# Kernel optimization log

Hardware: AMD Instinct MI355X
Metric: run time of the kernel (lower is better)

The kernel has to match this reference:

```python
import jax, jax.numpy as jnp
import numpy as np

TAU = 1.0
K_TAU = 1.0
MAX_K = 64


def setup_inputs() -> dict:
    key = jax.random.key(0)
    ks = jax.random.split(key, 6)
    B, S, D, H = 8, 4096, 1024, 2048
    token_embeddings = jax.random.normal(ks[0], (B, S, D), dtype=jnp.float32)
    W1 = jax.random.normal(ks[1], (D, H), dtype=jnp.float32) * (1.0 / np.sqrt(D))
    b1 = jnp.zeros((H,), dtype=jnp.float32)
    W2 = jax.random.normal(ks[2], (H, 1), dtype=jnp.float32) * (1.0 / np.sqrt(H))
    b2 = jnp.zeros((1,), dtype=jnp.float32)
    k_logits = jax.random.normal(ks[3], (MAX_K,), dtype=jnp.float32) * 0.02
    return {"token_embeddings": token_embeddings, "W1": W1, "b1": b1,
            "W2": W2, "b2": b2, "k_logits": k_logits}


def _gumbel(rng, shape):
    u = jax.random.uniform(rng, shape, minval=1e-08, maxval=1.0 - 1e-08)
    return -jnp.log(-jnp.log(u))


def reference(token_embeddings, W1, b1, W2, b2, k_logits):
    B, S, D = token_embeddings.shape
    # scorer: Dense -> relu -> Dense(1), squeeze -> [B, S]
    h = jax.nn.relu(jnp.einsum('bsd,dh->bsh', token_embeddings, W1) + b1)
    importance_logits = (jnp.einsum('bsh,ho->bso', h, W2) + b2)[..., 0]

    rng = jax.random.key(42)  # training rng
    rng1, rng2 = jax.random.split(rng)

    # learnable-k selection (training branch)
    k_gumbel = _gumbel(rng1, k_logits.shape)
    k_soft = jax.nn.softmax((k_logits + k_gumbel) / K_TAU)
    expected_k = jnp.sum(k_soft * jnp.arange(1, MAX_K + 1, dtype=k_soft.dtype))
    k_selected = jnp.argmax(k_soft) + 1  # traced int scalar

    # gumbel-softmax hard top-k over tokens
    perturbed = importance_logits + _gumbel(rng2, importance_logits.shape)
    soft_mask = jax.nn.softmax(perturbed / TAU, axis=-1)  # [B, S]
    # rank of each token (0 = smallest); top-k == rank >= S - k
    rank = jnp.argsort(jnp.argsort(soft_mask, axis=-1), axis=-1)
    hard_mask = (rank >= S - k_selected).astype(soft_mask.dtype)
    selection_mask = jax.lax.stop_gradient(hard_mask - soft_mask) + soft_mask

    filtered_embeddings = token_embeddings * selection_mask[..., None]
    return filtered_embeddings, selection_mask, expected_k
```

## Files before the change

### kernel.cpp

```cpp
#include <hip/hip_runtime.h>
#include <stdint.h>

#define B_BATCH 8
#define S_SEQ   4096
#define D_DIM   1024
#define H_DIM   2048
#define M_TOK   (B_BATCH * S_SEQ)
#define MAXK    64
#define NSPLIT  2

typedef unsigned int u32;
typedef unsigned short u16;
typedef unsigned long long u64;
typedef __attribute__((ext_vector_type(8))) short short8;
typedef __attribute__((ext_vector_type(4))) float f32x4;

#define GLOBAL_AS __attribute__((address_space(1)))
#define LDS_AS    __attribute__((address_space(3)))


#define TF_ROUND(x0, x1, r) { x0 += x1; x1 = ((x1 << r) | (x1 >> (32 - r))); x1 ^= x0; }

__device__ __forceinline__ void tf2x32(u32 k0, u32 k1, u32 x0, u32 x1, u32& o0, u32& o1) {
  u32 k2 = k0 ^ k1 ^ 0x1BD11BDAu;
  x0 += k0; x1 += k1;
  TF_ROUND(x0, x1, 13) TF_ROUND(x0, x1, 15) TF_ROUND(x0, x1, 26) TF_ROUND(x0, x1, 6)
  x0 += k1; x1 += k2 + 1u;
  TF_ROUND(x0, x1, 17) TF_ROUND(x0, x1, 29) TF_ROUND(x0, x1, 16) TF_ROUND(x0, x1, 24)
  x0 += k2; x1 += k0 + 2u;
  TF_ROUND(x0, x1, 13) TF_ROUND(x0, x1, 15) TF_ROUND(x0, x1, 26) TF_ROUND(x0, x1, 6)
  x0 += k0; x1 += k1 + 3u;
  TF_ROUND(x0, x1, 17) TF_ROUND(x0, x1, 29) TF_ROUND(x0, x1, 16) TF_ROUND(x0, x1, 24)
  x0 += k1; x1 += k2 + 4u;
  TF_ROUND(x0, x1, 13) TF_ROUND(x0, x1, 15) TF_ROUND(x0, x1, 26) TF_ROUND(x0, x1, 6)
  x0 += k2; x1 += k0 + 5u;
  o0 = x0; o1 = x1;
}

__device__ __forceinline__ void jax_subkeys(u32& r1a, u32& r1b, u32& r2a, u32& r2b) {
  tf2x32(0u, 42u, 0u, 0u, r1a, r1b);
  tf2x32(0u, 42u, 0u, 1u, r2a, r2b);
}

__device__ __forceinline__ u32 jax_bits32(u32 ka, u32 kb, u32 i) {
  u32 o0, o1;
  tf2x32(ka, kb, 0u, i, o0, o1);
  return o0 ^ o1;
}

__device__ __forceinline__ float jax_uniform_from_bits(u32 bits) {
  float f = __uint_as_float((bits >> 9) | 0x3f800000u) - 1.0f;
  float r = f + 1e-8f;
  return fmaxf(1e-8f, r);
}

__device__ __forceinline__ float gumbel_from_bits(u32 bits) {
  float u = jax_uniform_from_bits(bits);
  return -logf(-logf(u));
}

__device__ __forceinline__ u32 ordf(float v) {
  u32 b = __float_as_uint(v);
  return (b & 0x80000000u) ? ~b : (b | 0x80000000u);
}

__device__ __forceinline__ u64 shflx64(u64 v, int m) {
  unsigned lo = (unsigned)v, hi = (unsigned)(v >> 32);
  lo = (unsigned)__shfl_xor((int)lo, m);
  hi = (unsigned)__shfl_xor((int)hi, m);
  return ((u64)hi << 32) | lo;
}


__device__ __forceinline__ u16 f2bf_rn(float x) {
  u32 u = __float_as_uint(x);
  u32 r = u + 0x7fffu + ((u >> 16) & 1u);
  return (u16)(r >> 16);
}

__device__ __forceinline__ void split1(float x, u16& h, u16& lo) {
  h = f2bf_rn(x);
  float hf = __uint_as_float(((u32)h) << 16);
  lo = f2bf_rn(x - hf);
}


__global__ __launch_bounds__(256) void split_a_kernel(const float* __restrict__ x,
                                                      u16* __restrict__ hi,
                                                      u16* __restrict__ lo) {
  const size_t i = ((size_t)blockIdx.x * 256 + threadIdx.x) * 4;
  float4 v = *(const float4*)(x + i);
  u16 h0, h1, h2, h3, l0, l1, l2, l3;
  split1(v.x, h0, l0); split1(v.y, h1, l1); split1(v.z, h2, l2); split1(v.w, h3, l3);
  u64 hv = (u64)h0 | ((u64)h1 << 16) | ((u64)h2 << 32) | ((u64)h3 << 48);
  u64 lv = (u64)l0 | ((u64)l1 << 16) | ((u64)l2 << 32) | ((u64)l3 << 48);
  *(u64*)(hi + i) = hv;
  *(u64*)(lo + i) = lv;
}

__global__ __launch_bounds__(256) void split_w1t_kernel(const float* __restrict__ W1,
                                                        u16* __restrict__ bhi,
                                                        u16* __restrict__ blo) {
  __shared__ float tile[32][33];
  const int tx = threadIdx.x & 31, ty = threadIdx.x >> 5;
  const int n0 = blockIdx.x * 32, k0 = blockIdx.y * 32;
  #pragma unroll
  for (int r = 0; r < 4; ++r)
    tile[ty + r * 8][tx] = W1[(size_t)(k0 + ty + r * 8) * H_DIM + n0 + tx];
  __syncthreads();
  #pragma unroll
  for (int r = 0; r < 4; ++r) {
    const int n = n0 + ty + r * 8, k = k0 + tx;
    u16 h, l;
    split1(tile[tx][ty + r * 8], h, l);
    bhi[(size_t)n * D_DIM + k] = h;
    blo[(size_t)n * D_DIM + k] = l;
  }
}


__device__ __forceinline__ void stage16(const u16* g, u16* l) {
  __builtin_amdgcn_global_load_lds((const GLOBAL_AS u32*)g, (LDS_AS u32*)l, 16, 0, 0);
}

__global__ __launch_bounds__(256, 2) void scorer_mfma(
    const u16* __restrict__ Ahi, const u16* __restrict__ Alo,
    const u16* __restrict__ Bhi, const u16* __restrict__ Blo,
    const float* __restrict__ b1, const float* __restrict__ W2,
    float* __restrict__ pl) {
  __shared__ u16 smem[4 * 128 * 32];
  u16* sAhi = smem;
  u16* sAlo = smem + 4096;
  u16* sBhi = smem + 8192;
  u16* sBlo = smem + 12288;

  const int tid = threadIdx.x;
  const int w = tid >> 6;
  const int l = tid & 63;
  const int m0 = blockIdx.x * 128;
  const int nyb = blockIdx.y;

  const int rl0 = w * 32 + (l >> 2);
  const int rl1 = rl0 + 16;
  const int kloc0 = (((l & 3) ^ ((rl0 >> 1) & 3)) << 3);
  const int kloc1 = (((l & 3) ^ ((rl1 >> 1) & 3)) << 3);
  const int lb0 = (w * 32) * 32;
  const int lb1 = (w * 32 + 16) * 32;

  int a_off[4], b_off[4];
  #pragma unroll
  for (int i = 0; i < 4; ++i) {
    int row = ((w & 1) << 6) + i * 16 + (l & 15);
    int slot = (l >> 4) ^ ((row >> 1) & 3);
    a_off[i] = row * 32 + slot * 8;
    int nrow = ((w >> 1) << 6) + i * 16 + (l & 15);
    int nslot = (l >> 4) ^ ((nrow >> 1) & 3);
    b_off[i] = nrow * 32 + nslot * 8;
  }

  float logit[4][4];
  #pragma unroll
  for (int i = 0; i < 4; ++i)
    #pragma unroll
    for (int r = 0; r < 4; ++r) logit[i][r] = 0.f;

  for (int t8 = 0; t8 < H_DIM / (128 * NSPLIT); ++t8) {
    const int n0 = nyb * (H_DIM / NSPLIT) + t8 * 128;
    f32x4 acc[4][4];
    #pragma unroll
    for (int i = 0; i < 4; ++i)
      #pragma unroll
      for (int j = 0; j < 4; ++j) acc[i][j] = (f32x4){0.f, 0.f, 0.f, 0.f};

    const u16* pA0h = Ahi + (size_t)(m0 + rl0) * D_DIM + kloc0;
    const u16* pA1h = Ahi + (size_t)(m0 + rl1) * D_DIM + kloc1;
    const u16* pA0l = Alo + (size_t)(m0 + rl0) * D_DIM + kloc0;
    const u16* pA1l = Alo + (size_t)(m0 + rl1) * D_DIM + kloc1;
    const u16* pB0h = Bhi + (size_t)(n0 + rl0) * D_DIM + kloc0;
    const u16* pB1h = Bhi + (size_t)(n0 + rl1) * D_DIM + kloc1;
    const u16* pB0l = Blo + (size_t)(n0 + rl0) * D_DIM + kloc0;
    const u16* pB1l = Blo + (size_t)(n0 + rl1) * D_DIM + kloc1;

    for (int k0 = 0; k0 < D_DIM; k0 += 32) {
      __syncthreads();
      stage16(pA0h, sAhi + lb0); stage16(pA1h, sAhi + lb1);
      stage16(pA0l, sAlo + lb0); stage16(pA1l, sAlo + lb1);
      stage16(pB0h, sBhi + lb0); stage16(pB1h, sBhi + lb1);
      stage16(pB0l, sBlo + lb0); stage16(pB1l, sBlo + lb1);
      pA0h += 32; pA1h += 32; pA0l += 32; pA1l += 32;
      pB0h += 32; pB1h += 32; pB0l += 32; pB1l += 32;
      __syncthreads();

      short8 ah[4], al[4], bh[4], bl[4];
      #pragma unroll
      for (int i = 0; i < 4; ++i) {
        ah[i] = *(const short8*)(sAhi + a_off[i]);
        al[i] = *(const short8*)(sAlo + a_off[i]);
        bh[i] = *(const short8*)(sBhi + b_off[i]);
        bl[i] = *(const short8*)(sBlo + b_off[i]);
      }
      #pragma unroll
      for (int i = 0; i < 4; ++i)
        #pragma unroll
        for (int j = 0; j < 4; ++j) {
          acc[i][j] = __builtin_amdgcn_mfma_f32_16x16x32_bf16(ah[i], bh[j], acc[i][j], 0, 0, 0);
          acc[i][j] = __builtin_amdgcn_mfma_f32_16x16x32_bf16(ah[i], bl[j], acc[i][j], 0, 0, 0);
          acc[i][j] = __builtin_amdgcn_mfma_f32_16x16x32_bf16(al[i], bh[j], acc[i][j], 0, 0, 0);
        }
    }

    const int nb = n0 + ((w >> 1) << 6);
    #pragma unroll
    for (int j = 0; j < 4; ++j) {
      const int n = nb + j * 16 + (l & 15);
      const float b1v = b1[n];
      const float w2v = W2[n];
      #pragma unroll
      for (int i = 0; i < 4; ++i)
        #pragma unroll
        for (int r = 0; r < 4; ++r)
          logit[i][r] += fmaxf(acc[i][j][r] + b1v, 0.f) * w2v;
    }
  }

  __syncthreads();
  float* red = (float*)smem;
  const int col = (l & 15) + ((w >> 1) << 4);
  #pragma unroll
  for (int i = 0; i < 4; ++i)
    #pragma unroll
    for (int r = 0; r < 4; ++r) {
      const int m = ((w & 1) << 6) + i * 16 + ((l >> 4) << 2) + r;
      red[m * 33 + col] = logit[i][r];
    }
  __syncthreads();
  if (tid < 128) {
    float s = 0.f;
    #pragma unroll
    for (int x = 0; x < 32; ++x) s += red[tid * 33 + x];
    pl[(size_t)nyb * M_TOK + m0 + tid] = s;
  }
}


__global__ __launch_bounds__(256) void scorer_kernel(
    const float* __restrict__ emb, const float* __restrict__ W1,
    const float* __restrict__ b1, const float* __restrict__ W2,
    const float* __restrict__ b2, float* __restrict__ pert) {
  __shared__ float As[16][68];
  __shared__ float Bs[16][132];
  __shared__ float red[64][17];

  const int tid = threadIdx.x;
  const int tx = tid & 15;
  const int ty = tid >> 4;
  const int m0 = blockIdx.x * 64;
  const int at = tid >> 2;
  const int ac = (tid & 3) << 2;
  const int br = tid >> 4;
  const int bc = (tid & 15) << 3;

  float logit[4] = {0.f, 0.f, 0.f, 0.f};

  for (int n0 = 0; n0 < H_DIM; n0 += 128) {
    float acc[4][8];
    #pragma unroll
    for (int i = 0; i < 4; i++)
      #pragma unroll
      for (int j = 0; j < 8; j++) acc[i][j] = 0.f;

    for (int k0 = 0; k0 < D_DIM; k0 += 16) {
      float4 av  = *(const float4*)(emb + (size_t)(m0 + at) * D_DIM + (k0 + ac));
      float4 bv0 = *(const float4*)(W1 + (size_t)(k0 + br) * H_DIM + (n0 + bc));
      float4 bv1 = *(const float4*)(W1 + (size_t)(k0 + br) * H_DIM + (n0 + bc) + 4);
      __syncthreads();
      As[ac + 0][at] = av.x; As[ac + 1][at] = av.y;
      As[ac + 2][at] = av.z; As[ac + 3][at] = av.w;
      *(float4*)&Bs[br][bc]     = bv0;
      *(float4*)&Bs[br][bc + 4] = bv1;
      __syncthreads();
      #pragma unroll
      for (int k = 0; k < 16; k++) {
        float4 a   = *(const float4*)&As[k][ty << 2];
        float4 b0  = *(const float4*)&Bs[k][tx << 3];
        float4 b1v = *(const float4*)&Bs[k][(tx << 3) + 4];
        float aa[4] = {a.x, a.y, a.z, a.w};
        float bb[8] = {b0.x, b0.y, b0.z, b0.w, b1v.x, b1v.y, b1v.z, b1v.w};
        #pragma unroll
        for (int i = 0; i < 4; i++)
          #pragma unroll
          for (int j = 0; j < 8; j++)
            acc[i][j] = fmaf(aa[i], bb[j], acc[i][j]);
      }
    }
    float4 c0 = *(const float4*)(b1 + n0 + (tx << 3));
    float4 c1 = *(const float4*)(b1 + n0 + (tx << 3) + 4);
    float4 w0 = *(const float4*)(W2 + n0 + (tx << 3));
    float4 w1 = *(const float4*)(W2 + n0 + (tx << 3) + 4);
    float cb[8] = {c0.x, c0.y, c0.z, c0.w, c1.x, c1.y, c1.z, c1.w};
    float wb[8] = {w0.x, w0.y, w0.z, w0.w, w1.x, w1.y, w1.z, w1.w};
    #pragma unroll
    for (int i = 0; i < 4; i++)
      #pragma unroll
      for (int j = 0; j < 8; j++) {
        float h = fmaxf(acc[i][j] + cb[j], 0.f);
        logit[i] = fmaf(h, wb[j], logit[i]);
      }
  }

  __syncthreads();
  #pragma unroll
  for (int i = 0; i < 4; i++) red[(ty << 2) + i][tx] = logit[i];
  __syncthreads();

  if (tid < 64) {
    float s = 0.f;
    #pragma unroll
    for (int x = 0; x < 16; x++) s += red[tid][x];
    s += b2[0];
    int t = m0 + tid;
    u32 r1a, r1b, r2a, r2b;
    jax_subkeys(r1a, r1b, r2a, r2b);
    pert[t] = s + gumbel_from_bits(jax_bits32(r2a, r2b, (u32)t));
  }
}


template <bool FROM_PL>
__device__ __forceinline__ void topk_body(const float* kl, const float* pl,
                                          const float* b2, float* mask,
                                          float* expk) {
  const int r = blockIdx.x;
  const int tid = threadIdx.x;
  const int w = tid >> 6, l = tid & 63;
  __shared__ int ksel_sh;
  __shared__ int cnt[2][4];

  u32 r1a, r1b, r2a, r2b;
  jax_subkeys(r1a, r1b, r2a, r2b);

  if (tid < 64) {
    float p = kl[l] + gumbel_from_bits(jax_bits32(r1a, r1b, (u32)l));
    u64 kkey = ((u64)ordf(p) << 32) | (unsigned)(63 - l);
    #pragma unroll
    for (int off = 32; off >= 1; off >>= 1) {
      u64 o = shflx64(kkey, off);
      if (o > kkey) kkey = o;
    }
    if (l == 0) ksel_sh = 64 - (int)(kkey & 0xffffffffu);
    if (r == 0) {
      float m = p;
      #pragma unroll
      for (int off = 32; off >= 1; off >>= 1) m = fmaxf(m, __shfl_xor(m, off));
      float e = expf(p - m);
      float s = e;
      #pragma unroll
      for (int off = 32; off >= 1; off >>= 1) s += __shfl_xor(s, off);
      float v = (e / s) * (float)(l + 1);
      #pragma unroll
      for (int off = 32; off >= 1; off >>= 1) v += __shfl_xor(v, off);
      if (l == 0) expk[0] = v;
    }
  }
  __syncthreads();
  const int k = ksel_sh;
  const float b2v = FROM_PL ? b2[0] : 0.f;

  u64 keys[16];
  #pragma unroll
  for (int j = 0; j < 16; j++) {
    int s = tid + (j << 8);
    int t = (r << 12) + s;
    float v;
    if (FROM_PL) {
      float acc = pl[t];
      #pragma unroll
      for (int q = 1; q < NSPLIT; ++q) acc += pl[(size_t)q * M_TOK + t];
      v = acc + b2v + gumbel_from_bits(jax_bits32(r2a, r2b, (u32)t));
    } else {
      v = mask[t];
    }
    keys[j] = ((u64)ordf(v) << 12) | (unsigned)s;
  }

  u64 lo = 0ull, hi = (1ull << 44) - 1ull;
  int it = 0;
  while (lo < hi) {
    const u64 mid = (lo + hi + 1ull) >> 1;
    int c = 0;
    #pragma unroll
    for (int j = 0; j < 16; j++) c += (keys[j] >= mid) ? 1 : 0;
    #pragma unroll
    for (int off = 32; off >= 1; off >>= 1) c += __shfl_xor(c, off);
    const int buf = it & 1;
    if (l == 0) cnt[buf][w] = c;
    __syncthreads();
    const int tot = cnt[buf][0] + cnt[buf][1] + cnt[buf][2] + cnt[buf][3];
    if (tot >= k) lo = mid; else hi = mid - 1ull;
    ++it;
  }
  const u64 thresh = lo;

  #pragma unroll
  for (int j = 0; j < 16; j++) {
    int s = tid + (j << 8);
    mask[(r << 12) + s] = (keys[j] >= thresh) ? 1.0f : 0.0f;
  }
}

__global__ __launch_bounds__(256) void topk_pl_kernel(const float* __restrict__ kl,
                                                      const float* __restrict__ pl,
                                                      const float* __restrict__ b2,
                                                      float* __restrict__ mask,
                                                      float* __restrict__ expk) {
  topk_body<true>(kl, pl, b2, mask, expk);
}

__global__ __launch_bounds__(256) void topk_kernel(const float* __restrict__ kl,
                                                   float* __restrict__ mask,
                                                   float* __restrict__ expk) {
  topk_body<false>(kl, nullptr, nullptr, mask, expk);
}


__global__ __launch_bounds__(256) void filter_kernel(const float* __restrict__ emb,
                                                     const float* __restrict__ mask,
                                                     float* __restrict__ out) {
  const int t = blockIdx.x;
  const float mk = mask[t];
  const size_t base = (size_t)t * D_DIM + ((size_t)threadIdx.x << 2);
  float4 v = *(const float4*)(emb + base);
  *(float4*)(out + base) = make_float4(v.x * mk, v.y * mk, v.z * mk, v.w * mk);
}


extern "C" void kernel_launch(void* const* d_in, const int* in_sizes, int n_in,
                              void* d_out, int out_size, void* d_ws, size_t ws_size,
                              hipStream_t stream) {
  const float* emb = (const float*)d_in[0];
  const float* W1  = (const float*)d_in[1];
  const float* b1  = (const float*)d_in[2];
  const float* W2  = (const float*)d_in[3];
  const float* b2  = (const float*)d_in[4];
  const float* kl  = (const float*)d_in[5];
  float* out  = (float*)d_out;
  float* mask = out + (size_t)M_TOK * D_DIM;
  float* expk = mask + M_TOK;

  const size_t ws_need = (size_t)H_DIM * D_DIM * 2 * 2 + (size_t)NSPLIT * M_TOK * 4;

  if (ws_size >= ws_need) {
    u16* Ahi = (u16*)d_out;
    u16* Alo = Ahi + (size_t)M_TOK * D_DIM;
    u16* Bhi = (u16*)d_ws;
    u16* Blo = Bhi + (size_t)H_DIM * D_DIM;
    float* pl = (float*)(Blo + (size_t)H_DIM * D_DIM);

    split_a_kernel<<<M_TOK * D_DIM / 1024, 256, 0, stream>>>(emb, Ahi, Alo);
    split_w1t_kernel<<<dim3(H_DIM / 32, D_DIM / 32), 256, 0, stream>>>(W1, Bhi, Blo);
    scorer_mfma<<<dim3(M_TOK / 128, NSPLIT), 256, 0, stream>>>(Ahi, Alo, Bhi, Blo, b1, W2, pl);
    topk_pl_kernel<<<B_BATCH, 256, 0, stream>>>(kl, pl, b2, mask, expk);
  } else {
    scorer_kernel<<<M_TOK / 64, 256, 0, stream>>>(emb, W1, b1, W2, b2, mask);
    topk_kernel<<<B_BATCH, 256, 0, stream>>>(kl, mask, expk);
  }

  filter_kernel<<<M_TOK, 256, 0, stream>>>(emb, mask, out);
}
```

Baseline: 707.5 us.

## Double K-step per barrier and remap blocks across XCDs for L2 reuse

The scorer GEMM now stages 64 K-elements per loop iteration as two 32-wide sub-tiles, which halves the number of __syncthreads pairs and issues more loads per barrier. LDS use doubles to 64KB per block. The 2D grid becomes a 1D grid with an XCD-aware swizzle, so that blocks landing on the same XCD share A rows and the N-split half, with the aim of improving L2 locality. The larger LDS footprint may reduce occupancy below the two blocks per CU requested by the launch bounds.

```diff
diff --git a/kernel.cpp b/kernel.cpp
--- a/kernel.cpp
+++ b/kernel.cpp
@@ -128,17 +128,20 @@
     const u16* __restrict__ Bhi, const u16* __restrict__ Blo,
     const float* __restrict__ b1, const float* __restrict__ W2,
     float* __restrict__ pl) {
-  __shared__ u16 smem[4 * 128 * 32];
+  __shared__ u16 smem[8 * 128 * 32];
   u16* sAhi = smem;
-  u16* sAlo = smem + 4096;
-  u16* sBhi = smem + 8192;
-  u16* sBlo = smem + 12288;
+  u16* sAlo = smem + 8192;
+  u16* sBhi = smem + 16384;
+  u16* sBlo = smem + 24576;
 
   const int tid = threadIdx.x;
   const int w = tid >> 6;
   const int l = tid & 63;
-  const int m0 = blockIdx.x * 128;
-  const int nyb = blockIdx.y;
+
+  const int b = blockIdx.x;
+  const int xcd = b & 7;
+  const int nyb = xcd & 1;
+  const int m0 = ((b >> 3) * 4 + (xcd >> 1)) * 128;
 
   const int rl0 = w * 32 + (l >> 2);
   const int rl1 = rl0 + 16;
@@ -181,32 +184,41 @@
     const u16* pB0l = Blo + (size_t)(n0 + rl0) * D_DIM + kloc0;
     const u16* pB1l = Blo + (size_t)(n0 + rl1) * D_DIM + kloc1;
 
-    for (int k0 = 0; k0 < D_DIM; k0 += 32) {
+    for (int k0 = 0; k0 < D_DIM; k0 += 64) {
       __syncthreads();
-      stage16(pA0h, sAhi + lb0); stage16(pA1h, sAhi + lb1);
-      stage16(pA0l, sAlo + lb0); stage16(pA1l, sAlo + lb1);
-      stage16(pB0h, sBhi + lb0); stage16(pB1h, sBhi + lb1);
-      stage16(pB0l, sBlo + lb0); stage16(pB1l, sBlo + lb1);
-      pA0h += 32; pA1h += 32; pA0l += 32; pA1l += 32;
-      pB0h += 32; pB1h += 32; pB0l += 32; pB1l += 32;
+      #pragma unroll
+      for (int s = 0; s < 2; ++s) {
+        const int so = s * 4096;
+        const int sk = s * 32;
+        stage16(pA0h + sk, sAhi + so + lb0); stage16(pA1h + sk, sAhi + so + lb1);
+        stage16(pA0l + sk, sAlo + so + lb0); stage16(pA1l + sk, sAlo + so + lb1);
+        stage16(pB0h + sk, sBhi + so + lb0); stage16(pB1h + sk, sBhi + so + lb1);
+        stage16(pB0l + sk, sBlo + so + lb0); stage16(pB1l + sk, sBlo + so + lb1);
+      }
+      pA0h += 64; pA1h += 64; pA0l += 64; pA1l += 64;
+      pB0h += 64; pB1h += 64; pB0l += 64; pB1l += 64;
       __syncthreads();
 
-      short8 ah[4], al[4], bh[4], bl[4];
-      #pragma unroll
-      for (int i = 0; i < 4; ++i) {
-        ah[i] = *(const short8*)(sAhi + a_off[i]);
-        al[i] = *(const short8*)(sAlo + a_off[i]);
-        bh[i] = *(const short8*)(sBhi + b_off[i]);
-        bl[i] = *(const short8*)(sBlo + b_off[i]);
+      #pragma unroll
+      for (int s = 0; s < 2; ++s) {
+        const int so = s * 4096;
+        short8 ah[4], al[4], bh[4], bl[4];
+        #pragma unroll
+        for (int i = 0; i < 4; ++i) {
+          ah[i] = *(const short8*)(sAhi + so + a_off[i]);
+          al[i] = *(const short8*)(sAlo + so + a_off[i]);
+          bh[i] = *(const short8*)(sBhi + so + b_off[i]);
+          bl[i] = *(const short8*)(sBlo + so + b_off[i]);
+        }
+        #pragma unroll
+        for (int i = 0; i < 4; ++i)
+          #pragma unroll
+          for (int j = 0; j < 4; ++j) {
+            acc[i][j] = __builtin_amdgcn_mfma_f32_16x16x32_bf16(ah[i], bh[j], acc[i][j], 0, 0, 0);
+            acc[i][j] = __builtin_amdgcn_mfma_f32_16x16x32_bf16(ah[i], bl[j], acc[i][j], 0, 0, 0);
+            acc[i][j] = __builtin_amdgcn_mfma_f32_16x16x32_bf16(al[i], bh[j], acc[i][j], 0, 0, 0);
+          }
       }
-      #pragma unroll
-      for (int i = 0; i < 4; ++i)
-        #pragma unroll
-        for (int j = 0; j < 4; ++j) {
-          acc[i][j] = __builtin_amdgcn_mfma_f32_16x16x32_bf16(ah[i], bh[j], acc[i][j], 0, 0, 0);
-          acc[i][j] = __builtin_amdgcn_mfma_f32_16x16x32_bf16(ah[i], bl[j], acc[i][j], 0, 0, 0);
-          acc[i][j] = __builtin_amdgcn_mfma_f32_16x16x32_bf16(al[i], bh[j], acc[i][j], 0, 0, 0);
-        }
     }
 
     const int nb = n0 + ((w >> 1) << 6);
@@ -458,7 +470,7 @@
 
     split_a_kernel<<<M_TOK * D_DIM / 1024, 256, 0, stream>>>(emb, Ahi, Alo);
     split_w1t_kernel<<<dim3(H_DIM / 32, D_DIM / 32), 256, 0, stream>>>(W1, Bhi, Blo);
-    scorer_mfma<<<dim3(M_TOK / 128, NSPLIT), 256, 0, stream>>>(Ahi, Alo, Bhi, Blo, b1, W2, pl);
+    scorer_mfma<<<M_TOK / 128 * NSPLIT, 256, 0, stream>>>(Ahi, Alo, Bhi, Blo, b1, W2, pl);
     topk_pl_kernel<<<B_BATCH, 256, 0, stream>>>(kl, pl, b2, mask, expk);
   } else {
     scorer_kernel<<<M_TOK / 64, 256, 0, stream>>>(emb, W1, b1, W2, b2, mask);
```

Result: no change. 700.0 us (-1.1%).
